# Kernel tuning notes

Measured on AMD Instinct MI355X. Metric: run time of the kernel, lower is better.

The kernel has to match this reference:

```python
import jax, jax.numpy as jnp
import numpy as np

N_NODES = 100000


def _segment_mean(h, src, dst, n_nodes):
    # copy_u: gather source features along edges, then mean-reduce per dst node
    msg = h[src]                                             # [E, D]
    s = jax.ops.segment_sum(msg, dst, num_segments=n_nodes)  # [N, D]
    cnt = jax.ops.segment_sum(jnp.ones((src.shape[0],), h.dtype), dst,
                              num_segments=n_nodes)          # [N]
    return s / jnp.maximum(cnt, 1.0)[:, None]


def setup_inputs() -> dict:
    key = jax.random.key(0)
    k1, k2, k3, k4, k5 = jax.random.split(key, 5)
    in_feats, n_hidden, n_classes = 128, 128, 64
    n_edges = 1600000
    features = jax.random.normal(k1, (N_NODES, in_feats), dtype=jnp.float32)
    W1 = jax.random.normal(k2, (in_feats, n_hidden), dtype=jnp.float32) * (1.0 / np.sqrt(in_feats))
    b1 = jnp.zeros((n_hidden,), jnp.float32)
    W2 = jax.random.normal(k3, (n_hidden, n_classes), dtype=jnp.float32) * (1.0 / np.sqrt(n_hidden))
    b2 = jnp.zeros((n_classes,), jnp.float32)
    src = jax.random.randint(k4, (n_edges,), 0, N_NODES, dtype=jnp.int64)
    dst = jax.random.randint(k5, (n_edges,), 0, N_NODES, dtype=jnp.int64)
    return {"features": features, "W1": W1, "b1": b1, "W2": W2, "b2": b2,
            "src": src, "dst": dst}


def reference(features, W1, b1, W2, b2, src, dst):
    # Layer 0: mean aggregation -> Linear -> relu  (dropout p=0.0 is identity)
    h = _segment_mean(features, src, dst, N_NODES)
    h = jax.nn.relu(h @ W1 + b1)
    # Layer 1: mean aggregation -> Linear (no activation on output layer)
    h = _segment_mean(h, src, dst, N_NODES)
    h = h @ W2 + b2
    return h
```

## Files before the change

### kernel.cpp

```cpp
#include <hip/hip_runtime.h>

#define N_NODES 100000
#define D 128
#define NE 1600000
#define C_OUT 64
#define NB 391
#define SENT 100000
#define P2B 256
#define P2E 6250
#define SEGSTRIDE 6400

typedef _Float16 half8 __attribute__((ext_vector_type(8)));
typedef float floatx4 __attribute__((ext_vector_type(4)));


__device__ inline half8 shfl_xor_h8(half8 v, int mask) {
    union { half8 h; int i[4]; } u;
    u.h = v;
    u.i[0] = __shfl_xor(u.i[0], mask);
    u.i[1] = __shfl_xor(u.i[1], mask);
    u.i[2] = __shfl_xor(u.i[2], mask);
    u.i[3] = __shfl_xor(u.i[3], mask);
    return u.h;
}

__device__ inline void pack_one(const float* W, _Float16* Wp, int tid, int N) {
    int l = tid & 63, p = tid >> 6;
    int nt = p >> 2, kc = p & 3;
    int quad = l >> 4, c = l & 15;
    int n = nt * 16 + c;
    half8 h;
    #pragma unroll
    for (int j = 0; j < 8; ++j) {
        int k = kc * 32 + quad * 8 + j;
        h[j] = (_Float16)W[k * N + n];
    }
    *(half8*)(Wp + (size_t)p * 512 + l * 8) = h;
}

__global__ __launch_bounds__(1024) void k1_p2_setup(const int* __restrict__ src,
                                                    const int* __restrict__ dst,
                                                    unsigned* __restrict__ gwords,
                                                    int* __restrict__ ofsg,
                                                    const float* __restrict__ W1,
                                                    const float* __restrict__ W2,
                                                    _Float16* __restrict__ wp1,
                                                    _Float16* __restrict__ wp2,
                                                    int* __restrict__ t1s,
                                                    int* __restrict__ t2s) {
    if (blockIdx.x >= P2B) {
        const int blk = blockIdx.x - P2B;
        const int t = threadIdx.x;
        if (t < 256) {
            if (blk < 8) {
                pack_one(W1, wp1, blk * 256 + t, 128);
            } else if (blk < 12) {
                pack_one(W2, wp2, (blk - 8) * 256 + t, 64);
            } else {
                if (t < 64) t1s[t] = 0;
                else if (t < 96) t2s[t - 64] = 0;
            }
        }
        return;
    }

    __shared__ unsigned ebuf[P2E];
    __shared__ int hist[NB];
    __shared__ int ofs[NB + 1];
    __shared__ int cur[NB];
    __shared__ int wsum[8];
    const int t = threadIdx.x;
    const int base = blockIdx.x * P2E;

    for (int i = t; i < NB; i += 1024) hist[i] = 0;
    __syncthreads();

    unsigned w[7];
    int bk[7];
    #pragma unroll
    for (int r = 0; r < 7; ++r) {
        const int j = r * 1024 + t;
        if (j < P2E) {
            const int e = base + j;
            const int d = dst[e];
            w[r] = ((unsigned)(d & 255) << 20) | (unsigned)src[e];
            bk[r] = d >> 8;
            atomicAdd(&hist[bk[r]], 1);
        } else {
            bk[r] = -1;
        }
    }
    __syncthreads();

    int v = 0, incl = 0;
    if (t < 512) { v = (t < NB) ? hist[t] : 0; incl = v; }
    #pragma unroll
    for (int d = 1; d < 64; d <<= 1) {
        int y = __shfl_up(incl, d);
        if ((t & 63) >= d) incl += y;
    }
    if (t < 512 && (t & 63) == 63) wsum[t >> 6] = incl;
    __syncthreads();
    if (t < NB) {
        int ex = incl - v;
        const int wv = t >> 6;
        for (int j = 0; j < wv; ++j) ex += wsum[j];
        ofs[t] = ex;
        cur[t] = ex;
    }
    if (t == 0) ofs[NB] = P2E;
    __syncthreads();

    #pragma unroll
    for (int r = 0; r < 7; ++r) {
        if (bk[r] >= 0) {
            const int slot = atomicAdd(&cur[bk[r]], 1);
            ebuf[slot] = w[r];
        }
    }
    __syncthreads();

    unsigned* gout = gwords + (size_t)blockIdx.x * SEGSTRIDE;
    for (int i = t; i < P2E; i += 1024) gout[i] = ebuf[i];
    int* oout = ofsg + blockIdx.x * (NB + 1);
    for (int i = t; i < NB + 1; i += 1024) oout[i] = ofs[i];
}

#define K2_PSUM 391
__global__ __launch_bounds__(256) void k2_psum_gemm1(const int* __restrict__ ofsg,
                                                     int* __restrict__ btot,
                                                     const float* __restrict__ A,
                                                     const _Float16* __restrict__ Wp,
                                                     _Float16* __restrict__ outh) {
    __shared__ __align__(16) char smem[40960];
    const int t = threadIdx.x;

    if (blockIdx.x < K2_PSUM) {
        int* ws4 = (int*)smem;
        const int b = blockIdx.x;
        const int* row = ofsg + t * (NB + 1);
        int d = row[b + 1] - row[b];
        #pragma unroll
        for (int m = 1; m < 64; m <<= 1) d += __shfl_xor(d, m);
        if ((t & 63) == 0) ws4[t >> 6] = d;
        __syncthreads();
        if (t == 0) btot[b] = ws4[0] + ws4[1] + ws4[2] + ws4[3];
        return;
    }

    _Float16* Wl = (_Float16*)smem;
    _Float16* Al = (_Float16*)(smem + 32768);
    {
        const floatx4* s4 = (const floatx4*)Wp;
        floatx4* d4 = (floatx4*)Wl;
        #pragma unroll
        for (int i = 0; i < 8; ++i) d4[t + 256 * i] = s4[t + 256 * i];
    }
    const int lane = t & 63;
    const int wave = t >> 6;
    const int row0 = (blockIdx.x - K2_PSUM) * 128;

    floatx4 acc[8][2];
    #pragma unroll
    for (int mt = 0; mt < 8; ++mt)
        #pragma unroll
        for (int nt = 0; nt < 2; ++nt) acc[mt][nt] = (floatx4)0.0f;

    for (int kc = 0; kc < 4; ++kc) {
        __syncthreads();
        #pragma unroll
        for (int rep = 0; rep < 2; ++rep) {
            int p = rep * 256 + t;
            int r = p >> 2, quad = p & 3;
            int row = row0 + r;
            if (row > N_NODES - 1) row = N_NODES - 1;
            const float4 x0 = *(const float4*)(A + (size_t)row * D + kc * 32 + quad * 8);
            const float4 x1 = *(const float4*)(A + (size_t)row * D + kc * 32 + quad * 8 + 4);
            half8 h;
            h[0] = (_Float16)x0.x; h[1] = (_Float16)x0.y;
            h[2] = (_Float16)x0.z; h[3] = (_Float16)x0.w;
            h[4] = (_Float16)x1.x; h[5] = (_Float16)x1.y;
            h[6] = (_Float16)x1.z; h[7] = (_Float16)x1.w;
            int mt = r >> 4, m = r & 15;
            *(half8*)(Al + mt * 512 + (quad * 16 + m) * 8) = h;
        }
        __syncthreads();
        const half8* Af = (const half8*)Al;
        const half8* Bf = (const half8*)Wl;
        half8 b0 = Bf[((wave * 2 + 0) * 4 + kc) * 64 + lane];
        half8 b1 = Bf[((wave * 2 + 1) * 4 + kc) * 64 + lane];
        #pragma unroll
        for (int mt = 0; mt < 8; ++mt) {
            half8 a = Af[mt * 64 + lane];
            acc[mt][0] = __builtin_amdgcn_mfma_f32_16x16x32_f16(a, b0, acc[mt][0], 0, 0, 0);
            acc[mt][1] = __builtin_amdgcn_mfma_f32_16x16x32_f16(a, b1, acc[mt][1], 0, 0, 0);
        }
    }

    const int quad = lane >> 4, cl = lane & 15;
    #pragma unroll
    for (int mt = 0; mt < 8; ++mt)
        #pragma unroll
        for (int nt = 0; nt < 2; ++nt) {
            int col = wave * 32 + nt * 16 + cl;
            #pragma unroll
            for (int i = 0; i < 4; ++i) {
                int row = row0 + mt * 16 + quad * 4 + i;
                if (row < N_NODES)
                    outh[(size_t)row * D + col] = (_Float16)acc[mt][nt][i];
            }
        }
}

__global__ __launch_bounds__(256) void p3_finalize(const unsigned* __restrict__ gwords,
                                                   const int* __restrict__ ofsg,
                                                   const int* __restrict__ btot,
                                                   int* __restrict__ ptrp,
                                                   int* __restrict__ pcnt,
                                                   float* __restrict__ inv,
                                                   int* __restrict__ csr) {
    __shared__ unsigned wbuf[8192];
    __shared__ int lcnt[256];
    __shared__ int lofs[256];
    __shared__ int ws4[4];
    __shared__ int cursor;
    const int b = blockIdx.x;
    const int t = threadIdx.x;
    if (t == 0) cursor = 0;
    lcnt[t] = 0;

    int s = 0;
    for (int i = t; i < b; i += 256) s += btot[i];
    #pragma unroll
    for (int m = 1; m < 64; m <<= 1) s += __shfl_xor(s, m);
    if ((t & 63) == 0) ws4[t >> 6] = s;
    __syncthreads();
    const int bb = ws4[0] + ws4[1] + ws4[2] + ws4[3];
    const int pad_base = bb + 1792 * b;

    for (int blk = t; blk < P2B; blk += 256) {
        const int* row = ofsg + blk * (NB + 1);
        const int a = row[b];
        const int len = row[b + 1] - a;
        if (len > 0) {
            const int o = atomicAdd(&cursor, len);
            if (o + len <= 8192) {
                const unsigned* sseg = gwords + (size_t)blk * SEGSTRIDE + a;
                for (int j = 0; j < len; ++j) {
                    const unsigned w = sseg[j];
                    wbuf[o + j] = w;
                    atomicAdd(&lcnt[(w >> 20) & 255], 1);
                }
            }
        }
    }
    __syncthreads();

    const int tot = cursor;
    const int v = lcnt[t];
    const int pc = (v + 7) & ~7;
    int incl = pc;
    #pragma unroll
    for (int d = 1; d < 64; d <<= 1) {
        int y = __shfl_up(incl, d);
        if ((t & 63) >= d) incl += y;
    }
    __syncthreads();
    if ((t & 63) == 63) ws4[t >> 6] = incl;
    __syncthreads();
    int ex = incl - pc;
    {
        const int wv = t >> 6;
        for (int j = 0; j < wv; ++j) ex += ws4[j];
    }

    const int node = b * 256 + t;
    if (node < N_NODES) {
        ptrp[node] = pad_base + ex;
        pcnt[node] = pc;
        inv[node] = 1.0f / fmaxf((float)v, 1.0f);
    }
    for (int j = v; j < pc; ++j) csr[pad_base + ex + j] = SENT;

    __syncthreads();
    lofs[t] = ex;
    __syncthreads();
    for (int i = t; i < tot; i += 256) {
        const unsigned w = wbuf[i];
        const int pos = atomicAdd(&lofs[(w >> 20) & 255], 1);
        csr[pad_base + pos] = (int)(w & 0xFFFFF);
    }
}

__global__ __launch_bounds__(256) void k4_agg_gemm2(const _Float16* __restrict__ f,
                                                    const int* __restrict__ ptrp,
                                                    const int* __restrict__ pcnt,
                                                    const int* __restrict__ csr,
                                                    const float* __restrict__ inv,
                                                    const float* __restrict__ bias,
                                                    const _Float16* __restrict__ Wp,
                                                    _Float16* __restrict__ outh) {
    __shared__ __align__(16) _Float16 Wl[8192];
    __shared__ __align__(16) _Float16 h1t[16 * 136];
    const int t = threadIdx.x;
    {
        const floatx4* s4 = (const floatx4*)Wp;
        floatx4* d4 = (floatx4*)Wl;
        #pragma unroll
        for (int i = 0; i < 4; ++i) d4[t + 256 * i] = s4[t + 256 * i];
    }
    const int wave = t >> 6;
    const int lane = t & 63;
    const int q = lane & 15, hf = lane >> 4;
    const half8* f8 = (const half8*)f;

    for (int it = 0; it < 4; ++it) {
        const int r = wave * 4 + it;
        const int n = blockIdx.x * 16 + r;
        const int begin = ptrp[n];
        const int end = begin + pcnt[n];
        const float iv = inv[n];

        half8 acc0 = {0, 0, 0, 0, 0, 0, 0, 0};
        half8 acc1 = {0, 0, 0, 0, 0, 0, 0, 0};
        for (int base = begin; base < end; base += 64) {
            const int m = min(64, end - base);
            int edge = (lane < m) ? csr[base + lane] : SENT;
            int i = 0;
            for (; i + 16 <= m; i += 16) {
                int s0 = __shfl(edge, i + hf);
                int s1 = __shfl(edge, i + 4 + hf);
                int s2 = __shfl(edge, i + 8 + hf);
                int s3 = __shfl(edge, i + 12 + hf);
                half8 v0 = f8[(size_t)s0 * 16 + q];
                half8 v1 = f8[(size_t)s1 * 16 + q];
                half8 v2 = f8[(size_t)s2 * 16 + q];
                half8 v3 = f8[(size_t)s3 * 16 + q];
                acc0 += v0;
                acc1 += v1;
                acc0 += v2;
                acc1 += v3;
            }
            if (i < m) {
                int s0 = __shfl(edge, i + hf);
                int s1 = __shfl(edge, i + 4 + hf);
                half8 v0 = f8[(size_t)s0 * 16 + q];
                half8 v1 = f8[(size_t)s1 * 16 + q];
                acc0 += v0;
                acc1 += v1;
            }
        }
        acc0 += acc1;
        acc0 += shfl_xor_h8(acc0, 16);
        acc0 += shfl_xor_h8(acc0, 32);
        if (hf == 0) {
            const float4 b0 = ((const float4*)bias)[q * 2];
            const float4 b1v = ((const float4*)bias)[q * 2 + 1];
            half8 o;
            o[0] = (_Float16)fmaxf((float)acc0[0] * iv + b0.x, 0.f);
            o[1] = (_Float16)fmaxf((float)acc0[1] * iv + b0.y, 0.f);
            o[2] = (_Float16)fmaxf((float)acc0[2] * iv + b0.z, 0.f);
            o[3] = (_Float16)fmaxf((float)acc0[3] * iv + b0.w, 0.f);
            o[4] = (_Float16)fmaxf((float)acc0[4] * iv + b1v.x, 0.f);
            o[5] = (_Float16)fmaxf((float)acc0[5] * iv + b1v.y, 0.f);
            o[6] = (_Float16)fmaxf((float)acc0[6] * iv + b1v.z, 0.f);
            o[7] = (_Float16)fmaxf((float)acc0[7] * iv + b1v.w, 0.f);
            *(half8*)(h1t + r * 136 + q * 8) = o;
        }
    }
    __syncthreads();

    floatx4 acc = (floatx4)0.0f;
    #pragma unroll
    for (int kc = 0; kc < 4; ++kc) {
        half8 a = *(const half8*)(h1t + (lane & 15) * 136 + kc * 32 + (lane >> 4) * 8);
        half8 b = ((const half8*)Wl)[(wave * 4 + kc) * 64 + lane];
        acc = __builtin_amdgcn_mfma_f32_16x16x32_f16(a, b, acc, 0, 0, 0);
    }
    const int quad = lane >> 4, cl = lane & 15;
    const int col = wave * 16 + cl;
    #pragma unroll
    for (int i = 0; i < 4; ++i) {
        const int row = blockIdx.x * 16 + quad * 4 + i;
        outh[(size_t)row * C_OUT + col] = (_Float16)acc[i];
    }
}

__global__ __launch_bounds__(256) void agg64h(const _Float16* __restrict__ f,
                                              const int* __restrict__ ptrp,
                                              const int* __restrict__ pcnt,
                                              const int* __restrict__ csr,
                                              const float* __restrict__ inv,
                                              const float* __restrict__ bias,
                                              float* __restrict__ out) {
    const int wave = threadIdx.x >> 6;
    const int lane = threadIdx.x & 63;
    const int q = lane & 7, hf = lane >> 3;
    const int n = blockIdx.x * 4 + wave;
    const int begin = ptrp[n];
    const int end = begin + pcnt[n];
    const float iv = inv[n];
    const half8* f8 = (const half8*)f;

    half8 acc0 = {0, 0, 0, 0, 0, 0, 0, 0};
    half8 acc1 = {0, 0, 0, 0, 0, 0, 0, 0};
    for (int base = begin; base < end; base += 64) {
        const int m = min(64, end - base);
        int edge = (lane < m) ? csr[base + lane] : SENT;
        int i = 0;
        for (; i + 32 <= m; i += 32) {
            int s0 = __shfl(edge, i + hf);
            int s1 = __shfl(edge, i + 8 + hf);
            int s2 = __shfl(edge, i + 16 + hf);
            int s3 = __shfl(edge, i + 24 + hf);
            half8 v0 = f8[(size_t)s0 * 8 + q];
            half8 v1 = f8[(size_t)s1 * 8 + q];
            half8 v2 = f8[(size_t)s2 * 8 + q];
            half8 v3 = f8[(size_t)s3 * 8 + q];
            acc0 += v0;
            acc1 += v1;
            acc0 += v2;
            acc1 += v3;
        }
        if (i + 16 <= m) {
            int s0 = __shfl(edge, i + hf);
            int s1 = __shfl(edge, i + 8 + hf);
            half8 v0 = f8[(size_t)s0 * 8 + q];
            half8 v1 = f8[(size_t)s1 * 8 + q];
            acc0 += v0;
            acc1 += v1;
            i += 16;
        }
        if (i < m) {
            int s = __shfl(edge, i + hf);
            acc0 += f8[(size_t)s * 8 + q];
        }
    }
    acc0 += acc1;
    acc0 += shfl_xor_h8(acc0, 8);
    acc0 += shfl_xor_h8(acc0, 16);
    acc0 += shfl_xor_h8(acc0, 32);
    if (hf == 0) {
        const float4 b0 = ((const float4*)bias)[q * 2];
        const float4 b1 = ((const float4*)bias)[q * 2 + 1];
        float4 o0, o1;
        o0.x = (float)acc0[0] * iv + b0.x;
        o0.y = (float)acc0[1] * iv + b0.y;
        o0.z = (float)acc0[2] * iv + b0.z;
        o0.w = (float)acc0[3] * iv + b0.w;
        o1.x = (float)acc0[4] * iv + b1.x;
        o1.y = (float)acc0[5] * iv + b1.y;
        o1.z = (float)acc0[6] * iv + b1.z;
        o1.w = (float)acc0[7] * iv + b1.w;
        ((float4*)out)[(size_t)n * 16 + q * 2] = o0;
        ((float4*)out)[(size_t)n * 16 + q * 2 + 1] = o1;
    }
}

extern "C" void kernel_launch(void* const* d_in, const int* in_sizes, int n_in,
                              void* d_out, int out_size, void* d_ws, size_t ws_size,
                              hipStream_t stream) {
    const float* features = (const float*)d_in[0];
    const float* W1 = (const float*)d_in[1];
    const float* b1 = (const float*)d_in[2];
    const float* W2 = (const float*)d_in[3];
    const float* b2 = (const float*)d_in[4];
    const int* src = (const int*)d_in[5];
    const int* dst = (const int*)d_in[6];
    float* out = (float*)d_out;

    char* ws = (char*)d_ws;
    int*      ofsg  = (int*)(ws + 512L * 4);
    int*      btot  = (int*)(ws + 100864L * 4);
    int*      ptrp  = (int*)(ws + 125952L * 4);
    int*      pcnt  = (int*)(ws + 225952L * 4);
    float*    inv   = (float*)(ws + 325952L * 4);
    int*      csr   = (int*)(ws + 425952L * 4);
    unsigned* gwords= (unsigned*)(ws + 2825952L * 4);
    _Float16* wp1   = (_Float16*)(ws + 4464352L * 4);
    _Float16* wp2   = (_Float16*)(ws + 4472544L * 4);
    _Float16* t1h   = (_Float16*)(ws + 4476640L * 4);
    _Float16* t2h   = (_Float16*)(ws + 17276704L * 4);

    k1_p2_setup<<<P2B + 13, 1024, 0, stream>>>(src, dst, gwords, ofsg, W1, W2, wp1, wp2,
                                               (int*)(t1h + (size_t)SENT * 128),
                                               (int*)(t2h + (size_t)SENT * 64));
    k2_psum_gemm1<<<K2_PSUM + 782, 256, 0, stream>>>(ofsg, btot, features, wp1, t1h);
    p3_finalize<<<NB, 256, 0, stream>>>(gwords, ofsg, btot, ptrp, pcnt, inv, csr);
    k4_agg_gemm2<<<N_NODES / 16, 256, 0, stream>>>(t1h, ptrp, pcnt, csr, inv, b1, wp2, t2h);
    agg64h<<<N_NODES / 4, 256, 0, stream>>>(t2h, ptrp, pcnt, csr, inv, b2, out);
}
```

Measured before the change: 233.6 us.

## Slice layer-1 features into column slabs, split aggregation from GEMM2, fuse finalize into GEMM1

```diff
diff --git a/kernel.cpp b/kernel.cpp
--- a/kernel.cpp
+++ b/kernel.cpp
@@ -9,6 +9,7 @@
 #define P2B 256
 #define P2E 6250
 #define SEGSTRIDE 6400
+#define SLICE_STRIDE ((size_t)100001 * 16)
 
 typedef _Float16 half8 __attribute__((ext_vector_type(8)));
 typedef float floatx4 __attribute__((ext_vector_type(4)));
@@ -46,7 +47,7 @@
                                                     const float* __restrict__ W2,
                                                     _Float16* __restrict__ wp1,
                                                     _Float16* __restrict__ wp2,
-                                                    int* __restrict__ t1s,
+                                                    _Float16* __restrict__ t1s,
                                                     int* __restrict__ t2s) {
     if (blockIdx.x >= P2B) {
         const int blk = blockIdx.x - P2B;
@@ -57,8 +58,12 @@
             } else if (blk < 12) {
                 pack_one(W2, wp2, (blk - 8) * 256 + t, 64);
             } else {
-                if (t < 64) t1s[t] = 0;
-                else if (t < 96) t2s[t - 64] = 0;
+                if (t < 64) {
+                    const int s = t >> 3, j = t & 7;
+                    ((int*)t1s)[(size_t)s * (SLICE_STRIDE / 2) + 800000 + j] = 0;
+                } else if (t < 96) {
+                    t2s[t - 64] = 0;
+                }
             }
         }
         return;
@@ -126,25 +131,88 @@
     for (int i = t; i < NB + 1; i += 1024) oout[i] = ofs[i];
 }
 
-#define K2_PSUM 391
-__global__ __launch_bounds__(256) void k2_psum_gemm1(const int* __restrict__ ofsg,
-                                                     int* __restrict__ btot,
-                                                     const float* __restrict__ A,
-                                                     const _Float16* __restrict__ Wp,
-                                                     _Float16* __restrict__ outh) {
+__global__ __launch_bounds__(256) void k2_p3_gemm1(const unsigned* __restrict__ gwords,
+                                                   const int* __restrict__ ofsg,
+                                                   int* __restrict__ ptrp,
+                                                   int* __restrict__ pcnt,
+                                                   float* __restrict__ inv,
+                                                   int* __restrict__ csr,
+                                                   const float* __restrict__ A,
+                                                   const _Float16* __restrict__ Wp,
+                                                   _Float16* __restrict__ outh) {
     __shared__ __align__(16) char smem[40960];
     const int t = threadIdx.x;
 
-    if (blockIdx.x < K2_PSUM) {
-        int* ws4 = (int*)smem;
+    if (blockIdx.x < NB) {
+        unsigned* wbuf = (unsigned*)smem;
+        int* lcnt = (int*)(smem + 32768);
+        int* lofs = (int*)(smem + 33792);
+        int* ws4  = (int*)(smem + 34816);
+        int* curp = (int*)(smem + 34832);
         const int b = blockIdx.x;
-        const int* row = ofsg + t * (NB + 1);
-        int d = row[b + 1] - row[b];
-        #pragma unroll
-        for (int m = 1; m < 64; m <<= 1) d += __shfl_xor(d, m);
-        if ((t & 63) == 0) ws4[t >> 6] = d;
-        __syncthreads();
-        if (t == 0) btot[b] = ws4[0] + ws4[1] + ws4[2] + ws4[3];
+        if (t == 0) *curp = 0;
+        lcnt[t] = 0;
+
+        int sv = ofsg[t * (NB + 1) + b];
+        #pragma unroll
+        for (int m2 = 1; m2 < 64; m2 <<= 1) sv += __shfl_xor(sv, m2);
+        if ((t & 63) == 0) ws4[t >> 6] = sv;
+        __syncthreads();
+        const int bb = ws4[0] + ws4[1] + ws4[2] + ws4[3];
+        const int pad_base = bb + 1792 * b;
+
+        for (int blk = t; blk < P2B; blk += 256) {
+            const int* row = ofsg + blk * (NB + 1);
+            const int a = row[b];
+            const int len = row[b + 1] - a;
+            if (len > 0) {
+                const int o = atomicAdd(curp, len);
+                if (o + len <= 8192) {
+                    const unsigned* sseg = gwords + (size_t)blk * SEGSTRIDE + a;
+                    for (int j = 0; j < len; ++j) {
+                        const unsigned w = sseg[j];
+                        wbuf[o + j] = w;
+                        atomicAdd(&lcnt[(w >> 20) & 255], 1);
+                    }
+                }
+            }
+        }
+        __syncthreads();
+
+        const int tot = *curp;
+        const int v = lcnt[t];
+        const int pc = (v + 7) & ~7;
+        int incl = pc;
+        #pragma unroll
+        for (int d = 1; d < 64; d <<= 1) {
+            int y = __shfl_up(incl, d);
+            if ((t & 63) >= d) incl += y;
+        }
+        __syncthreads();
+        if ((t & 63) == 63) ws4[t >> 6] = incl;
+        __syncthreads();
+        int ex = incl - pc;
+        {
+            const int wv = t >> 6;
+            for (int j = 0; j < wv; ++j) ex += ws4[j];
+        }
+
+        const int node = b * 256 + t;
+        if (node < N_NODES) {
+            ptrp[node] = pad_base + ex;
+            pcnt[node] = pc;
+            inv[node] = 1.0f / fmaxf((float)v, 1.0f);
+        }
+        for (int j = v; j < pc; ++j) csr[pad_base + ex + j] = SENT;
+
+        __syncthreads();
+        lofs[t] = ex;
+        __syncthreads();
+        for (int i = t; i < tot; i += 256) {
+            const unsigned w = wbuf[i];
+            const int pos = atomicAdd(&lofs[(w >> 20) & 255], 1);
+            csr[pad_base + pos] = (int)(w & 0xFFFFF);
+        }
         return;
     }
 
@@ -158,7 +226,7 @@
     }
     const int lane = t & 63;
     const int wave = t >> 6;
-    const int row0 = (blockIdx.x - K2_PSUM) * 128;
+    const int row0 = (blockIdx.x - NB) * 128;
 
     floatx4 acc[8][2];
     #pragma unroll
@@ -202,106 +270,70 @@
     for (int mt = 0; mt < 8; ++mt)
         #pragma unroll
         for (int nt = 0; nt < 2; ++nt) {
-            int col = wave * 32 + nt * 16 + cl;
+            _Float16* sb = outh + (size_t)(wave * 2 + nt) * SLICE_STRIDE;
             #pragma unroll
             for (int i = 0; i < 4; ++i) {
                 int row = row0 + mt * 16 + quad * 4 + i;
                 if (row < N_NODES)
-                    outh[(size_t)row * D + col] = (_Float16)acc[mt][nt][i];
+                    sb[(size_t)row * 16 + cl] = (_Float16)acc[mt][nt][i];
             }
         }
 }
 
-__global__ __launch_bounds__(256) void p3_finalize(const unsigned* __restrict__ gwords,
-                                                   const int* __restrict__ ofsg,
-                                                   const int* __restrict__ btot,
-                                                   int* __restrict__ ptrp,
-                                                   int* __restrict__ pcnt,
-                                                   float* __restrict__ inv,
-                                                   int* __restrict__ csr) {
-    __shared__ unsigned wbuf[8192];
-    __shared__ int lcnt[256];
-    __shared__ int lofs[256];
-    __shared__ int ws4[4];
-    __shared__ int cursor;
-    const int b = blockIdx.x;
-    const int t = threadIdx.x;
-    if (t == 0) cursor = 0;
-    lcnt[t] = 0;
-
-    int s = 0;
-    for (int i = t; i < b; i += 256) s += btot[i];
-    #pragma unroll
-    for (int m = 1; m < 64; m <<= 1) s += __shfl_xor(s, m);
-    if ((t & 63) == 0) ws4[t >> 6] = s;
-    __syncthreads();
-    const int bb = ws4[0] + ws4[1] + ws4[2] + ws4[3];
-    const int pad_base = bb + 1792 * b;
-
-    for (int blk = t; blk < P2B; blk += 256) {
-        const int* row = ofsg + blk * (NB + 1);
-        const int a = row[b];
-        const int len = row[b + 1] - a;
-        if (len > 0) {
-            const int o = atomicAdd(&cursor, len);
-            if (o + len <= 8192) {
-                const unsigned* sseg = gwords + (size_t)blk * SEGSTRIDE + a;
-                for (int j = 0; j < len; ++j) {
-                    const unsigned w = sseg[j];
-                    wbuf[o + j] = w;
-                    atomicAdd(&lcnt[(w >> 20) & 255], 1);
-                }
-            }
-        }
-    }
-    __syncthreads();
-
-    const int tot = cursor;
-    const int v = lcnt[t];
-    const int pc = (v + 7) & ~7;
-    int incl = pc;
-    #pragma unroll
-    for (int d = 1; d < 64; d <<= 1) {
-        int y = __shfl_up(incl, d);
-        if ((t & 63) >= d) incl += y;
-    }
-    __syncthreads();
-    if ((t & 63) == 63) ws4[t >> 6] = incl;
-    __syncthreads();
-    int ex = incl - pc;
-    {
-        const int wv = t >> 6;
-        for (int j = 0; j < wv; ++j) ex += ws4[j];
-    }
-
-    const int node = b * 256 + t;
-    if (node < N_NODES) {
-        ptrp[node] = pad_base + ex;
-        pcnt[node] = pc;
-        inv[node] = 1.0f / fmaxf((float)v, 1.0f);
-    }
-    for (int j = v; j < pc; ++j) csr[pad_base + ex + j] = SENT;
-
-    __syncthreads();
-    lofs[t] = ex;
-    __syncthreads();
-    for (int i = t; i < tot; i += 256) {
-        const unsigned w = wbuf[i];
-        const int pos = atomicAdd(&lofs[(w >> 20) & 255], 1);
-        csr[pad_base + pos] = (int)(w & 0xFFFFF);
-    }
-}
-
-__global__ __launch_bounds__(256) void k4_agg_gemm2(const _Float16* __restrict__ f,
+__global__ __launch_bounds__(256) void k3_agg_slice(const _Float16* __restrict__ t1s,
                                                     const int* __restrict__ ptrp,
                                                     const int* __restrict__ pcnt,
                                                     const int* __restrict__ csr,
                                                     const float* __restrict__ inv,
                                                     const float* __restrict__ bias,
-                                                    const _Float16* __restrict__ Wp,
-                                                    _Float16* __restrict__ outh) {
+                                                    _Float16* __restrict__ h1h) {
+    const int s = blockIdx.x & 7;
+    const int g = blockIdx.x >> 3;
+    const int t = threadIdx.x;
+    const int wave = t >> 6, lane = t & 63;
+    const int G = lane >> 4;
+    const int P = lane & 15;
+    const int chunk = P & 1;
+    const int n = g * 16 + wave * 4 + G;
+    const int begin = ptrp[n];
+    const int end = begin + pcnt[n];
+    const float iv = inv[n];
+    const half8* fs = (const half8*)(t1s + (size_t)s * SLICE_STRIDE);
+
+    half8 acc = {0, 0, 0, 0, 0, 0, 0, 0};
+    for (int base = begin; base < end; base += 16) {
+        const int m = min(16, end - base);
+        int edge = (P < m) ? csr[base + P] : SENT;
+        #pragma unroll 2
+        for (int i = 0; i < m; i += 8) {
+            int srn = __shfl(edge, (lane & 48) + i + (P >> 1));
+            acc += fs[(size_t)srn * 2 + chunk];
+        }
+    }
+    acc += shfl_xor_h8(acc, 2);
+    acc += shfl_xor_h8(acc, 4);
+    acc += shfl_xor_h8(acc, 8);
+    if (P < 2) {
+        const float4 b0 = ((const float4*)bias)[s * 4 + chunk * 2];
+        const float4 b1 = ((const float4*)bias)[s * 4 + chunk * 2 + 1];
+        half8 o;
+        o[0] = (_Float16)fmaxf((float)acc[0] * iv + b0.x, 0.f);
+        o[1] = (_Float16)fmaxf((float)acc[1] * iv + b0.y, 0.f);
+        o[2] = (_Float16)fmaxf((float)acc[2] * iv + b0.z, 0.f);
+        o[3] = (_Float16)fmaxf((float)acc[3] * iv + b0.w, 0.f);
+        o[4] = (_Float16)fmaxf((float)acc[4] * iv + b1.x, 0.f);
+        o[5] = (_Float16)fmaxf((float)acc[5] * iv + b1.y, 0.f);
+        o[6] = (_Float16)fmaxf((float)acc[6] * iv + b1.z, 0.f);
+        o[7] = (_Float16)fmaxf((float)acc[7] * iv + b1.w, 0.f);
+        *(half8*)(h1h + (size_t)n * 128 + s * 16 + chunk * 8) = o;
+    }
+}
+
+__global__ __launch_bounds__(256) void gemm2(const _Float16* __restrict__ Ah,
+                                             const _Float16* __restrict__ Wp,
+                                             _Float16* __restrict__ outh) {
     __shared__ __align__(16) _Float16 Wl[8192];
-    __shared__ __align__(16) _Float16 h1t[16 * 136];
+    __shared__ __align__(16) _Float16 Al[4096];
     const int t = threadIdx.x;
     {
         const floatx4* s4 = (const floatx4*)Wp;
@@ -309,81 +341,47 @@
         #pragma unroll
         for (int i = 0; i < 4; ++i) d4[t + 256 * i] = s4[t + 256 * i];
     }
+    const int lane = t & 63;
     const int wave = t >> 6;
-    const int lane = t & 63;
-    const int q = lane & 15, hf = lane >> 4;
-    const half8* f8 = (const half8*)f;
-
-    for (int it = 0; it < 4; ++it) {
-        const int r = wave * 4 + it;
-        const int n = blockIdx.x * 16 + r;
-        const int begin = ptrp[n];
-        const int end = begin + pcnt[n];
-        const float iv = inv[n];
-
-        half8 acc0 = {0, 0, 0, 0, 0, 0, 0, 0};
-        half8 acc1 = {0, 0, 0, 0, 0, 0, 0, 0};
-        for (int base = begin; base < end; base += 64) {
-            const int m = min(64, end - base);
-            int edge = (lane < m) ? csr[base + lane] : SENT;
-            int i = 0;
-            for (; i + 16 <= m; i += 16) {
-                int s0 = __shfl(edge, i + hf);
-                int s1 = __shfl(edge, i + 4 + hf);
-                int s2 = __shfl(edge, i + 8 + hf);
-                int s3 = __shfl(edge, i + 12 + hf);
-                half8 v0 = f8[(size_t)s0 * 16 + q];
-                half8 v1 = f8[(size_t)s1 * 16 + q];
-                half8 v2 = f8[(size_t)s2 * 16 + q];
-                half8 v3 = f8[(size_t)s3 * 16 + q];
-                acc0 += v0;
-                acc1 += v1;
-                acc0 += v2;
-                acc1 += v3;
-            }
-            if (i < m) {
-                int s0 = __shfl(edge, i + hf);
-                int s1 = __shfl(edge, i + 4 + hf);
-                half8 v0 = f8[(size_t)s0 * 16 + q];
-                half8 v1 = f8[(size_t)s1 * 16 + q];
-                acc0 += v0;
-                acc1 += v1;
-            }
-        }
-        acc0 += acc1;
-        acc0 += shfl_xor_h8(acc0, 16);
-        acc0 += shfl_xor_h8(acc0, 32);
-        if (hf == 0) {
-            const float4 b0 = ((const float4*)bias)[q * 2];
-            const float4 b1v = ((const float4*)bias)[q * 2 + 1];
-            half8 o;
-            o[0] = (_Float16)fmaxf((float)acc0[0] * iv + b0.x, 0.f);
-            o[1] = (_Float16)fmaxf((float)acc0[1] * iv + b0.y, 0.f);
-            o[2] = (_Float16)fmaxf((float)acc0[2] * iv + b0.z, 0.f);
-            o[3] = (_Float16)fmaxf((float)acc0[3] * iv + b0.w, 0.f);
-            o[4] = (_Float16)fmaxf((float)acc0[4] * iv + b1v.x, 0.f);
-            o[5] = (_Float16)fmaxf((float)acc0[5] * iv + b1v.y, 0.f);
-            o[6] = (_Float16)fmaxf((float)acc0[6] * iv + b1v.z, 0.f);
-            o[7] = (_Float16)fmaxf((float)acc0[7] * iv + b1v.w, 0.f);
-            *(half8*)(h1t + r * 136 + q * 8) = o;
-        }
-    }
-    __syncthreads();
-
-    floatx4 acc = (floatx4)0.0f;
-    #pragma unroll
+    const int row0 = blockIdx.x * 128;
+
+    floatx4 acc[8];
+    #pragma unroll
+    for (int mt = 0; mt < 8; ++mt) acc[mt] = (floatx4)0.0f;
+
     for (int kc = 0; kc < 4; ++kc) {
-        half8 a = *(const half8*)(h1t + (lane & 15) * 136 + kc * 32 + (lane >> 4) * 8);
-        half8 b = ((const half8*)Wl)[(wave * 4 + kc) * 64 + lane];
-        acc = __builtin_amdgcn_mfma_f32_16x16x32_f16(a, b, acc, 0, 0, 0);
-    }
+        __syncthreads();
+        #pragma unroll
+        for (int rep = 0; rep < 2; ++rep) {
+            int p = rep * 256 + t;
+            int r = p >> 2, quad = p & 3;
+            int row = row0 + r;
+            if (row > N_NODES - 1) row = N_NODES - 1;
+            half8 h = *(const half8*)(Ah + (size_t)row * D + kc * 32 + quad * 8);
+            int mt = r >> 4, m = r & 15;
+            *(half8*)(Al + mt * 512 + (quad * 16 + m) * 8) = h;
+        }
+        __syncthreads();
+        const half8* Af = (const half8*)Al;
+        const half8* Bf = (const half8*)Wl;
+        half8 b = Bf[(wave * 4 + kc) * 64 + lane];
+        #pragma unroll
+        for (int mt = 0; mt < 8; ++mt) {
+            half8 a = Af[mt * 64 + lane];
+            acc[mt] = __builtin_amdgcn_mfma_f32_16x16x32_f16(a, b, acc[mt], 0, 0, 0);
+        }
+    }
+
     const int quad = lane >> 4, cl = lane & 15;
     const int col = wave * 16 + cl;
     #pragma unroll
-    for (int i = 0; i < 4; ++i) {
-        const int row = blockIdx.x * 16 + quad * 4 + i;
-        outh[(size_t)row * C_OUT + col] = (_Float16)acc[i];
-    }
+    for (int mt = 0; mt < 8; ++mt)
+        #pragma unroll
+        for (int i = 0; i < 4; ++i) {
+            int row = row0 + mt * 16 + quad * 4 + i;
+            if (row < N_NODES)
+                outh[(size_t)row * C_OUT + col] = (_Float16)acc[mt][i];
+        }
 }
 
 __global__ __launch_bounds__(256) void agg64h(const _Float16* __restrict__ f,
@@ -471,7 +469,6 @@
 
     char* ws = (char*)d_ws;
     int*      ofsg  = (int*)(ws + 512L * 4);
-    int*      btot  = (int*)(ws + 100864L * 4);
     int*      ptrp  = (int*)(ws + 125952L * 4);
     int*      pcnt  = (int*)(ws + 225952L * 4);
     float*    inv   = (float*)(ws + 325952L * 4);
@@ -479,14 +476,15 @@
     unsigned* gwords= (unsigned*)(ws + 2825952L * 4);
     _Float16* wp1   = (_Float16*)(ws + 4464352L * 4);
     _Float16* wp2   = (_Float16*)(ws + 4472544L * 4);
-    _Float16* t1h   = (_Float16*)(ws + 4476640L * 4);
+    _Float16* t1s   = (_Float16*)(ws + 4476640L * 4);
+    _Float16* h1h   = (_Float16*)(ws + 10876704L * 4);
     _Float16* t2h   = (_Float16*)(ws + 17276704L * 4);
 
     k1_p2_setup<<<P2B + 13, 1024, 0, stream>>>(src, dst, gwords, ofsg, W1, W2, wp1, wp2,
-                                               (int*)(t1h + (size_t)SENT * 128),
-                                               (int*)(t2h + (size_t)SENT * 64));
-    k2_psum_gemm1<<<K2_PSUM + 782, 256, 0, stream>>>(ofsg, btot, features, wp1, t1h);
-    p3_finalize<<<NB, 256, 0, stream>>>(gwords, ofsg, btot, ptrp, pcnt, inv, csr);
-    k4_agg_gemm2<<<N_NODES / 16, 256, 0, stream>>>(t1h, ptrp, pcnt, csr, inv, b1, wp2, t2h);
+                                               t1s, (int*)(t2h + (size_t)SENT * 64));
+    k2_p3_gemm1<<<NB + 782, 256, 0, stream>>>(gwords, ofsg, ptrp, pcnt, inv, csr,
+                                              features, wp1, t1s);
+    k3_agg_slice<<<(N_NODES / 16) * 8, 256, 0, stream>>>(t1s, ptrp, pcnt, csr, inv, b1, h1h);
+    gemm2<<<(N_NODES + 127) / 128, 256, 0, stream>>>(h1h, wp2, t2h);
     agg64h<<<N_NODES / 4, 256, 0, stream>>>(t2h, ptrp, pcnt, csr, inv, b2, out);
 }
```

Measured after the change: 276.3 us. +18.2%, slower.

## Replace two-pass bucketed CSR build with global atomic count and scatter

Applied to the files above, without the earlier changes.

```diff
diff --git a/kernel.cpp b/kernel.cpp
--- a/kernel.cpp
+++ b/kernel.cpp
@@ -6,13 +6,10 @@
 #define C_OUT 64
 #define NB 391
 #define SENT 100000
-#define P2B 256
-#define P2E 6250
-#define SEGSTRIDE 6400
+#define CSR_CAP 2400000
 
 typedef _Float16 half8 __attribute__((ext_vector_type(8)));
 typedef float floatx4 __attribute__((ext_vector_type(4)));
-
 
 __device__ inline half8 shfl_xor_h8(half8 v, int mask) {
     union { half8 h; int i[4]; } u;
@@ -38,113 +35,132 @@
     *(half8*)(Wp + (size_t)p * 512 + l * 8) = h;
 }
 
-__global__ __launch_bounds__(1024) void k1_p2_setup(const int* __restrict__ src,
-                                                    const int* __restrict__ dst,
-                                                    unsigned* __restrict__ gwords,
-                                                    int* __restrict__ ofsg,
-                                                    const float* __restrict__ W1,
-                                                    const float* __restrict__ W2,
-                                                    _Float16* __restrict__ wp1,
-                                                    _Float16* __restrict__ wp2,
-                                                    int* __restrict__ t1s,
-                                                    int* __restrict__ t2s) {
-    if (blockIdx.x >= P2B) {
-        const int blk = blockIdx.x - P2B;
-        const int t = threadIdx.x;
-        if (t < 256) {
-            if (blk < 8) {
-                pack_one(W1, wp1, blk * 256 + t, 128);
-            } else if (blk < 12) {
-                pack_one(W2, wp2, (blk - 8) * 256 + t, 64);
-            } else {
-                if (t < 64) t1s[t] = 0;
-                else if (t < 96) t2s[t - 64] = 0;
-            }
-        }
+#define CSRF_BLOCKS 2344
+#define GCNT_BLOCKS 98
+__global__ __launch_bounds__(256) void kA_init(const float* __restrict__ W1,
+                                               const float* __restrict__ W2,
+                                               _Float16* __restrict__ wp1,
+                                               _Float16* __restrict__ wp2,
+                                               int* __restrict__ t1s,
+                                               int* __restrict__ t2s,
+                                               int* __restrict__ csr,
+                                               int* __restrict__ gcnt) {
+    const int blk = blockIdx.x;
+    const int t = threadIdx.x;
+    if (blk < CSRF_BLOCKS) {
+        const int idx = blk * 1024 + t * 4;
+        if (idx + 4 <= CSR_CAP)
+            *(int4*)(csr + idx) = make_int4(SENT, SENT, SENT, SENT);
         return;
     }
-
-    __shared__ unsigned ebuf[P2E];
-    __shared__ int hist[NB];
-    __shared__ int ofs[NB + 1];
-    __shared__ int cur[NB];
-    __shared__ int wsum[8];
+    if (blk < CSRF_BLOCKS + GCNT_BLOCKS) {
+        const int idx = (blk - CSRF_BLOCKS) * 1024 + t * 4;
+        if (idx + 4 <= N_NODES)
+            *(int4*)(gcnt + idx) = make_int4(0, 0, 0, 0);
+        return;
+    }
+    const int r = blk - CSRF_BLOCKS - GCNT_BLOCKS;
+    if (r < 8) {
+        pack_one(W1, wp1, r * 256 + t, 128);
+    } else if (r < 12) {
+        pack_one(W2, wp2, (r - 8) * 256 + t, 64);
+    } else {
+        if (t < 64) t1s[t] = 0;
+        else if (t < 96) t2s[t - 64] = 0;
+    }
+}
+
+__global__ __launch_bounds__(256) void kB_count(const int* __restrict__ dst,
+                                                int* __restrict__ gcnt) {
+    const int base = blockIdx.x * 2048 + threadIdx.x;
+    #pragma unroll
+    for (int r = 0; r < 8; ++r) {
+        const int e = base + r * 256;
+        if (e < NE) atomicAdd(&gcnt[dst[e]], 1);
+    }
+}
+
+__global__ __launch_bounds__(256) void kC_bsum(const int* __restrict__ gcnt,
+                                               int* __restrict__ bsum) {
+    __shared__ int ws4[4];
+    const int b = blockIdx.x;
     const int t = threadIdx.x;
-    const int base = blockIdx.x * P2E;
-
-    for (int i = t; i < NB; i += 1024) hist[i] = 0;
+    const int node = b * 256 + t;
+    int v = (node < N_NODES) ? gcnt[node] : 0;
+    int pc = (v + 7) & ~7;
+    #pragma unroll
+    for (int m = 1; m < 64; m <<= 1) pc += __shfl_xor(pc, m);
+    if ((t & 63) == 0) ws4[t >> 6] = pc;
     __syncthreads();
-
-    unsigned w[7];
-    int bk[7];
-    #pragma unroll
-    for (int r = 0; r < 7; ++r) {
-        const int j = r * 1024 + t;
-        if (j < P2E) {
-            const int e = base + j;
-            const int d = dst[e];
-            w[r] = ((unsigned)(d & 255) << 20) | (unsigned)src[e];
-            bk[r] = d >> 8;
-            atomicAdd(&hist[bk[r]], 1);
-        } else {
-            bk[r] = -1;
-        }
-    }
+    if (t == 0) bsum[b] = ws4[0] + ws4[1] + ws4[2] + ws4[3];
+}
+
+__global__ __launch_bounds__(256) void kD_ptr(const int* __restrict__ gcnt,
+                                              const int* __restrict__ bsum,
+                                              int* __restrict__ ptrp,
+                                              int* __restrict__ pcnt,
+                                              float* __restrict__ inv,
+                                              int* __restrict__ cur) {
+    __shared__ int ws4[4];
+    const int b = blockIdx.x;
+    const int t = threadIdx.x;
+    const int lane = t & 63, wave = t >> 6;
+
+    int s0 = 0;
+    for (int i = t; i < b; i += 256) s0 += bsum[i];
+    #pragma unroll
+    for (int m = 1; m < 64; m <<= 1) s0 += __shfl_xor(s0, m);
+    if (lane == 0) ws4[wave] = s0;
     __syncthreads();
-
-    int v = 0, incl = 0;
-    if (t < 512) { v = (t < NB) ? hist[t] : 0; incl = v; }
+    const int base = ws4[0] + ws4[1] + ws4[2] + ws4[3];
+    __syncthreads();
+
+    const int node = b * 256 + t;
+    const int v = (node < N_NODES) ? gcnt[node] : 0;
+    const int pc = (v + 7) & ~7;
+    int incl = pc;
     #pragma unroll
     for (int d = 1; d < 64; d <<= 1) {
         int y = __shfl_up(incl, d);
-        if ((t & 63) >= d) incl += y;
-    }
-    if (t < 512 && (t & 63) == 63) wsum[t >> 6] = incl;
+        if (lane >= d) incl += y;
+    }
+    if (lane == 63) ws4[wave] = incl;
     __syncthreads();
-    if (t < NB) {
-        int ex = incl - v;
-        const int wv = t >> 6;
-        for (int j = 0; j < wv; ++j) ex += wsum[j];
-        ofs[t] = ex;
-        cur[t] = ex;
-    }
-    if (t == 0) ofs[NB] = P2E;
-    __syncthreads();
-
-    #pragma unroll
-    for (int r = 0; r < 7; ++r) {
-        if (bk[r] >= 0) {
-            const int slot = atomicAdd(&cur[bk[r]], 1);
-            ebuf[slot] = w[r];
-        }
-    }
-    __syncthreads();
-
-    unsigned* gout = gwords + (size_t)blockIdx.x * SEGSTRIDE;
-    for (int i = t; i < P2E; i += 1024) gout[i] = ebuf[i];
-    int* oout = ofsg + blockIdx.x * (NB + 1);
-    for (int i = t; i < NB + 1; i += 1024) oout[i] = ofs[i];
-}
-
-#define K2_PSUM 391
-__global__ __launch_bounds__(256) void k2_psum_gemm1(const int* __restrict__ ofsg,
-                                                     int* __restrict__ btot,
-                                                     const float* __restrict__ A,
-                                                     const _Float16* __restrict__ Wp,
-                                                     _Float16* __restrict__ outh) {
+    int ex = incl - pc;
+    for (int j = 0; j < wave; ++j) ex += ws4[j];
+
+    if (node < N_NODES) {
+        const int p = base + ex;
+        ptrp[node] = p;
+        pcnt[node] = pc;
+        inv[node] = 1.0f / fmaxf((float)v, 1.0f);
+        cur[node] = p;
+    }
+}
+
+#define KE_SCAT 782
+__global__ __launch_bounds__(256) void kE_scatter_gemm1(const int* __restrict__ src,
+                                                        const int* __restrict__ dst,
+                                                        int* __restrict__ cur,
+                                                        int* __restrict__ csr,
+                                                        const float* __restrict__ A,
+                                                        const _Float16* __restrict__ Wp,
+                                                        _Float16* __restrict__ outh) {
     __shared__ __align__(16) char smem[40960];
     const int t = threadIdx.x;
 
-    if (blockIdx.x < K2_PSUM) {
-        int* ws4 = (int*)smem;
-        const int b = blockIdx.x;
-        const int* row = ofsg + t * (NB + 1);
-        int d = row[b + 1] - row[b];
-        #pragma unroll
-        for (int m = 1; m < 64; m <<= 1) d += __shfl_xor(d, m);
-        if ((t & 63) == 0) ws4[t >> 6] = d;
-        __syncthreads();
-        if (t == 0) btot[b] = ws4[0] + ws4[1] + ws4[2] + ws4[3];
+    if (blockIdx.x < KE_SCAT) {
+        const int base = blockIdx.x * 2048 + t;
+        #pragma unroll
+        for (int r = 0; r < 8; ++r) {
+            const int e = base + r * 256;
+            if (e < NE) {
+                const int d = dst[e];
+                const int s = src[e];
+                const int pos = atomicAdd(&cur[d], 1);
+                csr[pos] = s;
+            }
+        }
         return;
     }
 
@@ -158,7 +174,7 @@
     }
     const int lane = t & 63;
     const int wave = t >> 6;
-    const int row0 = (blockIdx.x - K2_PSUM) * 128;
+    const int row0 = (blockIdx.x - KE_SCAT) * 128;
 
     floatx4 acc[8][2];
     #pragma unroll
@@ -212,87 +228,7 @@
         }
 }
 
-__global__ __launch_bounds__(256) void p3_finalize(const unsigned* __restrict__ gwords,
-                                                   const int* __restrict__ ofsg,
-                                                   const int* __restrict__ btot,
-                                                   int* __restrict__ ptrp,
-                                                   int* __restrict__ pcnt,
-                                                   float* __restrict__ inv,
-                                                   int* __restrict__ csr) {
-    __shared__ unsigned wbuf[8192];
-    __shared__ int lcnt[256];
-    __shared__ int lofs[256];
-    __shared__ int ws4[4];
-    __shared__ int cursor;
-    const int b = blockIdx.x;
-    const int t = threadIdx.x;
-    if (t == 0) cursor = 0;
-    lcnt[t] = 0;
-
-    int s = 0;
-    for (int i = t; i < b; i += 256) s += btot[i];
-    #pragma unroll
-    for (int m = 1; m < 64; m <<= 1) s += __shfl_xor(s, m);
-    if ((t & 63) == 0) ws4[t >> 6] = s;
-    __syncthreads();
-    const int bb = ws4[0] + ws4[1] + ws4[2] + ws4[3];
-    const int pad_base = bb + 1792 * b;
-
-    for (int blk = t; blk < P2B; blk += 256) {
-        const int* row = ofsg + blk * (NB + 1);
-        const int a = row[b];
-        const int len = row[b + 1] - a;
-        if (len > 0) {
-            const int o = atomicAdd(&cursor, len);
-            if (o + len <= 8192) {
-                const unsigned* sseg = gwords + (size_t)blk * SEGSTRIDE + a;
-                for (int j = 0; j < len; ++j) {
-                    const unsigned w = sseg[j];
-                    wbuf[o + j] = w;
-                    atomicAdd(&lcnt[(w >> 20) & 255], 1);
-                }
-            }
-        }
-    }
-    __syncthreads();
-
-    const int tot = cursor;
-    const int v = lcnt[t];
-    const int pc = (v + 7) & ~7;
-    int incl = pc;
-    #pragma unroll
-    for (int d = 1; d < 64; d <<= 1) {
-        int y = __shfl_up(incl, d);
-        if ((t & 63) >= d) incl += y;
-    }
-    __syncthreads();
-    if ((t & 63) == 63) ws4[t >> 6] = incl;
-    __syncthreads();
-    int ex = incl - pc;
-    {
-        const int wv = t >> 6;
-        for (int j = 0; j < wv; ++j) ex += ws4[j];
-    }
-
-    const int node = b * 256 + t;
-    if (node < N_NODES) {
-        ptrp[node] = pad_base + ex;
-        pcnt[node] = pc;
-        inv[node] = 1.0f / fmaxf((float)v, 1.0f);
-    }
-    for (int j = v; j < pc; ++j) csr[pad_base + ex + j] = SENT;
-
-    __syncthreads();
-    lofs[t] = ex;
-    __syncthreads();
-    for (int i = t; i < tot; i += 256) {
-        const unsigned w = wbuf[i];
-        const int pos = atomicAdd(&lofs[(w >> 20) & 255], 1);
-        csr[pad_base + pos] = (int)(w & 0xFFFFF);
-    }
-}
-
-__global__ __launch_bounds__(256) void k4_agg_gemm2(const _Float16* __restrict__ f,
+__global__ __launch_bounds__(256) void kF_agg_gemm2(const _Float16* __restrict__ f,
                                                     const int* __restrict__ ptrp,
                                                     const int* __restrict__ pcnt,
                                                     const int* __restrict__ csr,
@@ -386,13 +322,13 @@
     }
 }
 
-__global__ __launch_bounds__(256) void agg64h(const _Float16* __restrict__ f,
-                                              const int* __restrict__ ptrp,
-                                              const int* __restrict__ pcnt,
-                                              const int* __restrict__ csr,
-                                              const float* __restrict__ inv,
-                                              const float* __restrict__ bias,
-                                              float* __restrict__ out) {
+__global__ __launch_bounds__(256) void kG_agg64(const _Float16* __restrict__ f,
+                                                const int* __restrict__ ptrp,
+                                                const int* __restrict__ pcnt,
+                                                const int* __restrict__ csr,
+                                                const float* __restrict__ inv,
+                                                const float* __restrict__ bias,
+                                                float* __restrict__ out) {
     const int wave = threadIdx.x >> 6;
     const int lane = threadIdx.x & 63;
     const int q = lane & 7, hf = lane >> 3;
@@ -470,23 +406,27 @@
     float* out = (float*)d_out;
 
     char* ws = (char*)d_ws;
-    int*      ofsg  = (int*)(ws + 512L * 4);
-    int*      btot  = (int*)(ws + 100864L * 4);
+    int*      gcnt  = (int*)(ws + 512L * 4);
+    int*      bsum  = (int*)(ws + 101000L * 4);
     int*      ptrp  = (int*)(ws + 125952L * 4);
     int*      pcnt  = (int*)(ws + 225952L * 4);
     float*    inv   = (float*)(ws + 325952L * 4);
     int*      csr   = (int*)(ws + 425952L * 4);
-    unsigned* gwords= (unsigned*)(ws + 2825952L * 4);
+    int*      cur   = (int*)(ws + 2825952L * 4);
     _Float16* wp1   = (_Float16*)(ws + 4464352L * 4);
     _Float16* wp2   = (_Float16*)(ws + 4472544L * 4);
     _Float16* t1h   = (_Float16*)(ws + 4476640L * 4);
     _Float16* t2h   = (_Float16*)(ws + 17276704L * 4);
 
-    k1_p2_setup<<<P2B + 13, 1024, 0, stream>>>(src, dst, gwords, ofsg, W1, W2, wp1, wp2,
-                                               (int*)(t1h + (size_t)SENT * 128),
-                                               (int*)(t2h + (size_t)SENT * 64));
-    k2_psum_gemm1<<<K2_PSUM + 782, 256, 0, stream>>>(ofsg, btot, features, wp1, t1h);
-    p3_finalize<<<NB, 256, 0, stream>>>(gwords, ofsg, btot, ptrp, pcnt, inv, csr);
-    k4_agg_gemm2<<<N_NODES / 16, 256, 0, stream>>>(t1h, ptrp, pcnt, csr, inv, b1, wp2, t2h);
-    agg64h<<<N_NODES / 4, 256, 0, stream>>>(t2h, ptrp, pcnt, csr, inv, b2, out);
-}
+    kA_init<<<CSRF_BLOCKS + GCNT_BLOCKS + 13, 256, 0, stream>>>(
+        W1, W2, wp1, wp2,
+        (int*)(t1h + (size_t)SENT * 128), (int*)(t2h + (size_t)SENT * 64),
+        csr, gcnt);
+    kB_count<<<782, 256, 0, stream>>>(dst, gcnt);
+    kC_bsum<<<NB, 256, 0, stream>>>(gcnt, bsum);
+    kD_ptr<<<NB, 256, 0, stream>>>(gcnt, bsum, ptrp, pcnt, inv, cur);
+    kE_scatter_gemm1<<<KE_SCAT + 782, 256, 0, stream>>>(src, dst, cur, csr,
+                                                        features, wp1, t1h);
+    kF_agg_gemm2<<<N_NODES / 16, 256, 0, stream>>>(t1h, ptrp, pcnt, csr, inv, b1, wp2, t2h);
+    kG_agg64<<<N_NODES / 4, 256, 0, stream>>>(t2h, ptrp, pcnt, csr, inv, b2, out);
+}
```

After: 447.7 us. 1.92x slower.

## Fuse CSR finalize into GEMM1 launch using per-block prefix from segment offsets

Applied to the files above, without the earlier changes.

```diff
diff --git a/kernel.cpp b/kernel.cpp
--- a/kernel.cpp
+++ b/kernel.cpp
@@ -126,25 +126,103 @@
     for (int i = t; i < NB + 1; i += 1024) oout[i] = ofs[i];
 }
 
-#define K2_PSUM 391
-__global__ __launch_bounds__(256) void k2_psum_gemm1(const int* __restrict__ ofsg,
-                                                     int* __restrict__ btot,
-                                                     const float* __restrict__ A,
-                                                     const _Float16* __restrict__ Wp,
-                                                     _Float16* __restrict__ outh) {
+__global__ __launch_bounds__(256) void k2_p3_gemm1(const unsigned* __restrict__ gwords,
+                                                   const int* __restrict__ ofsg,
+                                                   int* __restrict__ ptrp,
+                                                   int* __restrict__ pcnt,
+                                                   float* __restrict__ inv,
+                                                   int* __restrict__ csr,
+                                                   const float* __restrict__ A,
+                                                   const _Float16* __restrict__ Wp,
+                                                   _Float16* __restrict__ outh) {
     __shared__ __align__(16) char smem[40960];
     const int t = threadIdx.x;
 
-    if (blockIdx.x < K2_PSUM) {
-        int* ws4 = (int*)smem;
+    if (blockIdx.x < NB) {
+        unsigned* wbuf = (unsigned*)smem;
+        int* sa   = (int*)(smem + 32768);
+        int* sl   = (int*)(smem + 33792);
+        int* so   = (int*)(smem + 34816);
+        int* lcnt = (int*)(smem + 35840);
+        int* lofs = (int*)(smem + 36864);
+        int* ws4  = (int*)(smem + 37888);
         const int b = blockIdx.x;
+        const int lane = t & 63, wave = t >> 6;
+
         const int* row = ofsg + t * (NB + 1);
-        int d = row[b + 1] - row[b];
-        #pragma unroll
-        for (int m = 1; m < 64; m <<= 1) d += __shfl_xor(d, m);
-        if ((t & 63) == 0) ws4[t >> 6] = d;
-        __syncthreads();
-        if (t == 0) btot[b] = ws4[0] + ws4[1] + ws4[2] + ws4[3];
+        const int a0 = row[b];
+        const int len = row[b + 1] - a0;
+        sa[t] = a0;
+        sl[t] = len;
+
+        int sv = a0;
+        #pragma unroll
+        for (int m2 = 1; m2 < 64; m2 <<= 1) sv += __shfl_xor(sv, m2);
+        if (lane == 0) ws4[wave] = sv;
+        __syncthreads();
+        const int pad_base = (ws4[0] + ws4[1] + ws4[2] + ws4[3]) + 1792 * b;
+        __syncthreads();
+
+        int incl = len;
+        #pragma unroll
+        for (int d = 1; d < 64; d <<= 1) {
+            int y = __shfl_up(incl, d);
+            if (lane >= d) incl += y;
+        }
+        if (lane == 63) ws4[wave] = incl;
+        lcnt[t] = 0;
+        __syncthreads();
+        int off = incl - len;
+        for (int j = 0; j < wave; ++j) off += ws4[j];
+        so[t] = off;
+        const int tot = min(ws4[0] + ws4[1] + ws4[2] + ws4[3], 8192);
+        __syncthreads();
+
+        const int grp = t >> 4, gl = t & 15;
+        for (int seg = grp; seg < P2B; seg += 16) {
+            const int sega = sa[seg];
+            const int segl = sl[seg];
+            const int sego = so[seg];
+            if (sego + segl > 8192) continue;
+            const unsigned* sp = gwords + (size_t)seg * SEGSTRIDE + sega;
+            for (int j = gl; j < segl; j += 16) {
+                const unsigned w = sp[j];
+                wbuf[sego + j] = w;
+                atomicAdd(&lcnt[(w >> 20) & 255], 1);
+            }
+        }
+        __syncthreads();
+
+        const int v = lcnt[t];
+        const int pc = (v + 7) & ~7;
+        int incl2 = pc;
+        #pragma unroll
+        for (int d = 1; d < 64; d <<= 1) {
+            int y = __shfl_up(incl2, d);
+            if (lane >= d) incl2 += y;
+        }
+        __syncthreads();
+        if (lane == 63) ws4[wave] = incl2;
+        __syncthreads();
+        int ex = incl2 - pc;
+        for (int j = 0; j < wave; ++j) ex += ws4[j];
+
+        const int node = b * 256 + t;
+        if (node < N_NODES) {
+            ptrp[node] = pad_base + ex;
+            pcnt[node] = pc;
+            inv[node] = 1.0f / fmaxf((float)v, 1.0f);
+        }
+        for (int j = v; j < pc; ++j) csr[pad_base + ex + j] = SENT;
+
+        __syncthreads();
+        lofs[t] = ex;
+        __syncthreads();
+        for (int i = t; i < tot; i += 256) {
+            const unsigned w = wbuf[i];
+            const int pos = atomicAdd(&lofs[(w >> 20) & 255], 1);
+            csr[pad_base + pos] = (int)(w & 0xFFFFF);
+        }
         return;
     }
 
@@ -158,7 +236,7 @@
     }
     const int lane = t & 63;
     const int wave = t >> 6;
-    const int row0 = (blockIdx.x - K2_PSUM) * 128;
+    const int row0 = (blockIdx.x - NB) * 128;
 
     floatx4 acc[8][2];
     #pragma unroll
@@ -212,87 +290,7 @@
         }
 }
 
-__global__ __launch_bounds__(256) void p3_finalize(const unsigned* __restrict__ gwords,
-                                                   const int* __restrict__ ofsg,
-                                                   const int* __restrict__ btot,
-                                                   int* __restrict__ ptrp,
-                                                   int* __restrict__ pcnt,
-                                                   float* __restrict__ inv,
-                                                   int* __restrict__ csr) {
-    __shared__ unsigned wbuf[8192];
-    __shared__ int lcnt[256];
-    __shared__ int lofs[256];
-    __shared__ int ws4[4];
-    __shared__ int cursor;
-    const int b = blockIdx.x;
-    const int t = threadIdx.x;
-    if (t == 0) cursor = 0;
-    lcnt[t] = 0;
-
-    int s = 0;
-    for (int i = t; i < b; i += 256) s += btot[i];
-    #pragma unroll
-    for (int m = 1; m < 64; m <<= 1) s += __shfl_xor(s, m);
-    if ((t & 63) == 0) ws4[t >> 6] = s;
-    __syncthreads();
-    const int bb = ws4[0] + ws4[1] + ws4[2] + ws4[3];
-    const int pad_base = bb + 1792 * b;
-
-    for (int blk = t; blk < P2B; blk += 256) {
-        const int* row = ofsg + blk * (NB + 1);
-        const int a = row[b];
-        const int len = row[b + 1] - a;
-        if (len > 0) {
-            const int o = atomicAdd(&cursor, len);
-            if (o + len <= 8192) {
-                const unsigned* sseg = gwords + (size_t)blk * SEGSTRIDE + a;
-                for (int j = 0; j < len; ++j) {
-                    const unsigned w = sseg[j];
-                    wbuf[o + j] = w;
-                    atomicAdd(&lcnt[(w >> 20) & 255], 1);
-                }
-            }
-        }
-    }
-    __syncthreads();
-
-    const int tot = cursor;
-    const int v = lcnt[t];
-    const int pc = (v + 7) & ~7;
-    int incl = pc;
-    #pragma unroll
-    for (int d = 1; d < 64; d <<= 1) {
-        int y = __shfl_up(incl, d);
-        if ((t & 63) >= d) incl += y;
-    }
-    __syncthreads();
-    if ((t & 63) == 63) ws4[t >> 6] = incl;
-    __syncthreads();
-    int ex = incl - pc;
-    {
-        const int wv = t >> 6;
-        for (int j = 0; j < wv; ++j) ex += ws4[j];
-    }
-
-    const int node = b * 256 + t;
-    if (node < N_NODES) {
-        ptrp[node] = pad_base + ex;
-        pcnt[node] = pc;
-        inv[node] = 1.0f / fmaxf((float)v, 1.0f);
-    }
-    for (int j = v; j < pc; ++j) csr[pad_base + ex + j] = SENT;
-
-    __syncthreads();
-    lofs[t] = ex;
-    __syncthreads();
-    for (int i = t; i < tot; i += 256) {
-        const unsigned w = wbuf[i];
-        const int pos = atomicAdd(&lofs[(w >> 20) & 255], 1);
-        csr[pad_base + pos] = (int)(w & 0xFFFFF);
-    }
-}
-
-__global__ __launch_bounds__(256) void k4_agg_gemm2(const _Float16* __restrict__ f,
+__global__ __launch_bounds__(256) void kF_agg_gemm2(const _Float16* __restrict__ f,
                                                     const int* __restrict__ ptrp,
                                                     const int* __restrict__ pcnt,
                                                     const int* __restrict__ csr,
@@ -386,13 +384,13 @@
     }
 }
 
-__global__ __launch_bounds__(256) void agg64h(const _Float16* __restrict__ f,
-                                              const int* __restrict__ ptrp,
-                                              const int* __restrict__ pcnt,
-                                              const int* __restrict__ csr,
-                                              const float* __restrict__ inv,
-                                              const float* __restrict__ bias,
-                                              float* __restrict__ out) {
+__global__ __launch_bounds__(256) void kG_agg64(const _Float16* __restrict__ f,
+                                                const int* __restrict__ ptrp,
+                                                const int* __restrict__ pcnt,
+                                                const int* __restrict__ csr,
+                                                const float* __restrict__ inv,
+                                                const float* __restrict__ bias,
+                                                float* __restrict__ out) {
     const int wave = threadIdx.x >> 6;
     const int lane = threadIdx.x & 63;
     const int q = lane & 7, hf = lane >> 3;
@@ -471,7 +469,6 @@
 
     char* ws = (char*)d_ws;
     int*      ofsg  = (int*)(ws + 512L * 4);
-    int*      btot  = (int*)(ws + 100864L * 4);
     int*      ptrp  = (int*)(ws + 125952L * 4);
     int*      pcnt  = (int*)(ws + 225952L * 4);
     float*    inv   = (float*)(ws + 325952L * 4);
@@ -485,8 +482,8 @@
     k1_p2_setup<<<P2B + 13, 1024, 0, stream>>>(src, dst, gwords, ofsg, W1, W2, wp1, wp2,
                                                (int*)(t1h + (size_t)SENT * 128),
                                                (int*)(t2h + (size_t)SENT * 64));
-    k2_psum_gemm1<<<K2_PSUM + 782, 256, 0, stream>>>(ofsg, btot, features, wp1, t1h);
-    p3_finalize<<<NB, 256, 0, stream>>>(gwords, ofsg, btot, ptrp, pcnt, inv, csr);
-    k4_agg_gemm2<<<N_NODES / 16, 256, 0, stream>>>(t1h, ptrp, pcnt, csr, inv, b1, wp2, t2h);
-    agg64h<<<N_NODES / 4, 256, 0, stream>>>(t2h, ptrp, pcnt, csr, inv, b2, out);
-}
+    k2_p3_gemm1<<<NB + 782, 256, 0, stream>>>(gwords, ofsg, ptrp, pcnt, inv, csr,
+                                              features, wp1, t1h);
+    kF_agg_gemm2<<<N_NODES / 16, 256, 0, stream>>>(t1h, ptrp, pcnt, csr, inv, b1, wp2, t2h);
+    kG_agg64<<<N_NODES / 4, 256, 0, stream>>>(t2h, ptrp, pcnt, csr, inv, b2, out);
+}
```

Result: faster. 227.4 us (-2.7%).
